# Kernel tuning notes

Hardware: AMD Instinct MI355X
Metric: run time of the kernel (lower is better)

Reference implementation:

```python
import jax, jax.numpy as jnp
import numpy as np


def setup_inputs() -> dict:
    key = jax.random.key(0)
    k1, k2 = jax.random.split(key)
    B, S, H = 8, 4096, 1024
    sequence_output = jax.random.normal(k1, (B, S, H), dtype=jnp.float32)
    # labels in {0,1}: no -100 padding so the mask-compaction has a static shape
    sent_token_mask = jax.random.randint(k2, (B, S), 0, 2, dtype=jnp.int64)
    return {"sequence_output": sequence_output, "sent_token_mask": sent_token_mask}


def reference(sequence_output, sent_token_mask):
    B, S, H = sequence_output.shape
    # mask compaction: all positions valid (labels in {0,1}), so it's a reshape
    sent_features = sequence_output.reshape(B * S, H)  # [B*S, H]

    labels = sent_token_mask  # [B, S]
    # seg_id assigned BEFORE processing each label; increments AFTER label==0
    inc = (labels == 0).astype(jnp.int32).reshape(B * S)
    within = jnp.cumsum(inc) - inc  # exclusive prefix sum of increments
    # extra increment at end of each example whose last label == 1
    extra = (labels[:, -1] == 1).astype(jnp.int32)  # [B]
    extra_off = jnp.cumsum(extra) - extra           # exclusive over examples
    topic_segment_ids = within.reshape(B, S) + extra_off[:, None]
    return sent_features, topic_segment_ids.reshape(B * S)
```

## Files before the change

### kernel.cpp

```cpp
#include <hip/hip_runtime.h>

constexpr int Bn  = 8;
constexpr int Sn  = 4096;
constexpr int Nn  = Bn * Sn;
constexpr int Hn  = 1024;
constexpr int TPB = 1024;
constexpr int PER = Nn / TPB;
constexpr int NW  = TPB / 64;

constexpr size_t FEAT_ELEMS = (size_t)Nn * Hn;
constexpr size_t FEAT_VEC4  = FEAT_ELEMS / 4;
constexpr int    VEC_PER_T  = 8;
constexpr int    COPY_BLOCKS = (int)(FEAT_VEC4 / ((size_t)TPB * VEC_PER_T));

__global__ __launch_bounds__(TPB) void fused_kernel(const float* __restrict__ seq,
                                                    const int* __restrict__ labels,
                                                    float* __restrict__ out) {
    if (blockIdx.x < COPY_BLOCKS) {
        const float4* __restrict__ src = reinterpret_cast<const float4*>(seq);
        float4* __restrict__ dst       = reinterpret_cast<float4*>(out);
        const size_t base   = (size_t)blockIdx.x * TPB + threadIdx.x;
        const size_t stride = (size_t)COPY_BLOCKS * TPB;
#pragma unroll
        for (int i = 0; i < VEC_PER_T; ++i) {
            const size_t idx = base + (size_t)i * stride;
            dst[idx] = src[idx];
        }
        return;
    }

    __shared__ int wave_sums[NW];
    __shared__ int extra_off_sh[Bn];

    float* __restrict__ seg_out = out + FEAT_ELEMS;

    const int tid  = threadIdx.x;
    const int lane = tid & 63;
    const int wave = tid >> 6;
    const int base = tid * PER;

    int inc[PER];
    int sum = 0;
    const int4* l4 = reinterpret_cast<const int4*>(labels + base);
#pragma unroll
    for (int i = 0; i < PER / 4; ++i) {
        int4 v = l4[i];
        inc[4 * i + 0] = (v.x == 0); sum += inc[4 * i + 0];
        inc[4 * i + 1] = (v.y == 0); sum += inc[4 * i + 1];
        inc[4 * i + 2] = (v.z == 0); sum += inc[4 * i + 2];
        inc[4 * i + 3] = (v.w == 0); sum += inc[4 * i + 3];
    }

    int incl = sum;
#pragma unroll
    for (int off = 1; off < 64; off <<= 1) {
        int u = __shfl_up(incl, off, 64);
        if (lane >= off) incl += u;
    }
    if (lane == 63) wave_sums[wave] = incl;

    if (tid == 0) {
        int acc = 0;
#pragma unroll
        for (int b = 0; b < Bn; ++b) {
            extra_off_sh[b] = acc;
            acc += (labels[b * Sn + Sn - 1] == 1);
        }
    }
    __syncthreads();

    if (wave == 0) {
        int v = (lane < NW) ? wave_sums[lane] : 0;
#pragma unroll
        for (int off = 1; off < NW; off <<= 1) {
            int u = __shfl_up(v, off, 64);
            if (lane >= off) v += u;
        }
        if (lane < NW) wave_sums[lane] = v;
    }
    __syncthreads();

    int excl = (wave ? wave_sums[wave - 1] : 0) + (incl - sum);
#pragma unroll
    for (int i = 0; i < PER; ++i) {
        int idx = base + i;
        seg_out[idx] = (float)(excl + extra_off_sh[idx >> 12]);
        excl += inc[i];
    }
}

extern "C" void kernel_launch(void* const* d_in, const int* in_sizes, int n_in,
                              void* d_out, int out_size, void* d_ws, size_t ws_size,
                              hipStream_t stream) {
    const float* seq    = (const float*)d_in[0];
    const int*   labels = (const int*)d_in[1];
    float*       out    = (float*)d_out;

    fused_kernel<<<COPY_BLOCKS + 1, TPB, 0, stream>>>(seq, labels, out);
}
```

Measured before the change: 243.2 us.

## Shrink blocks, use contiguous per-block copy chunks, reload labels in scan

Reduces the block size from 1024 to 256 threads and the per-thread copy work from 8 to 4 float4s, while giving each copy block a contiguous chunk instead of a grid-strided pattern. The scan block now sits at block 0 and re-reads labels rather than keeping a 32/128-entry inc array in registers. The aim is better occupancy and less register pressure. The trade-off is that the single scan block does 128 labels per thread serially, which may lengthen the tail.

```diff
diff --git a/kernel.cpp b/kernel.cpp
--- a/kernel.cpp
+++ b/kernel.cpp
@@ -4,28 +4,31 @@
 constexpr int Sn  = 4096;
 constexpr int Nn  = Bn * Sn;
 constexpr int Hn  = 1024;
-constexpr int TPB = 1024;
+
+constexpr int TPB = 256;
+constexpr int NW  = TPB / 64;
 constexpr int PER = Nn / TPB;
-constexpr int NW  = TPB / 64;
 
 constexpr size_t FEAT_ELEMS = (size_t)Nn * Hn;
 constexpr size_t FEAT_VEC4  = FEAT_ELEMS / 4;
-constexpr int    VEC_PER_T  = 8;
+constexpr int    VEC_PER_T  = 4;
 constexpr int    COPY_BLOCKS = (int)(FEAT_VEC4 / ((size_t)TPB * VEC_PER_T));
 
 __global__ __launch_bounds__(TPB) void fused_kernel(const float* __restrict__ seq,
                                                     const int* __restrict__ labels,
                                                     float* __restrict__ out) {
-    if (blockIdx.x < COPY_BLOCKS) {
+    if (blockIdx.x > 0) {
         const float4* __restrict__ src = reinterpret_cast<const float4*>(seq);
         float4* __restrict__ dst       = reinterpret_cast<float4*>(out);
-        const size_t base   = (size_t)blockIdx.x * TPB + threadIdx.x;
-        const size_t stride = (size_t)COPY_BLOCKS * TPB;
-#pragma unroll
-        for (int i = 0; i < VEC_PER_T; ++i) {
-            const size_t idx = base + (size_t)i * stride;
-            dst[idx] = src[idx];
-        }
+        const size_t base = (size_t)(blockIdx.x - 1) * (TPB * VEC_PER_T) + threadIdx.x;
+        float4 r0 = src[base + 0 * TPB];
+        float4 r1 = src[base + 1 * TPB];
+        float4 r2 = src[base + 2 * TPB];
+        float4 r3 = src[base + 3 * TPB];
+        dst[base + 0 * TPB] = r0;
+        dst[base + 1 * TPB] = r1;
+        dst[base + 2 * TPB] = r2;
+        dst[base + 3 * TPB] = r3;
         return;
     }
 
@@ -39,16 +42,12 @@
     const int wave = tid >> 6;
     const int base = tid * PER;
 
-    int inc[PER];
+    const int4* l4 = reinterpret_cast<const int4*>(labels + base);
     int sum = 0;
-    const int4* l4 = reinterpret_cast<const int4*>(labels + base);
 #pragma unroll
     for (int i = 0; i < PER / 4; ++i) {
         int4 v = l4[i];
-        inc[4 * i + 0] = (v.x == 0); sum += inc[4 * i + 0];
-        inc[4 * i + 1] = (v.y == 0); sum += inc[4 * i + 1];
-        inc[4 * i + 2] = (v.z == 0); sum += inc[4 * i + 2];
-        inc[4 * i + 3] = (v.w == 0); sum += inc[4 * i + 3];
+        sum += (v.x == 0) + (v.y == 0) + (v.z == 0) + (v.w == 0);
     }
 
     int incl = sum;
@@ -82,10 +81,17 @@
 
     int excl = (wave ? wave_sums[wave - 1] : 0) + (incl - sum);
 #pragma unroll
-    for (int i = 0; i < PER; ++i) {
-        int idx = base + i;
-        seg_out[idx] = (float)(excl + extra_off_sh[idx >> 12]);
-        excl += inc[i];
+    for (int i = 0; i < PER / 4; ++i) {
+        int4 v = l4[i];
+        int idx = base + 4 * i;
+        int eo  = extra_off_sh[idx >> 12];
+        seg_out[idx + 0] = (float)(excl + eo); excl += (v.x == 0);
+        eo = extra_off_sh[(idx + 1) >> 12];
+        seg_out[idx + 1] = (float)(excl + eo); excl += (v.y == 0);
+        eo = extra_off_sh[(idx + 2) >> 12];
+        seg_out[idx + 2] = (float)(excl + eo); excl += (v.z == 0);
+        eo = extra_off_sh[(idx + 3) >> 12];
+        seg_out[idx + 3] = (float)(excl + eo); excl += (v.w == 0);
     }
 }
 
```

Measured after the change: 229.6 us. 1.06x faster.
